# Kernel tuning notes

Hardware: AMD Instinct MI355X
Metric: run time of the kernel (lower is better)

The kernel has to match this reference:

```python
import jax, jax.numpy as jnp
import numpy as np

B, K, H, W = 16, 32, 28, 28   # batch, set size, image h, image w
HID, OUT = 64, 64             # hid_dim, out_dim
NOPS = 8                      # permutation-equivariant 3->3 pool/broadcast basis ops


def setup_inputs() -> dict:
    key = jax.random.key(0)
    ks = jax.random.split(key, 8)
    def p(k, shape, fan_in):
        return jax.random.normal(k, shape, jnp.float32) / np.float32(np.sqrt(fan_in))
    return dict(
        x=jax.random.normal(ks[0], (B, K, H, W), jnp.float32),
        conv1_w=p(ks[1], (32, 1, 3, 3), 9),
        conv1_b=jnp.zeros((32,), jnp.float32),
        conv2_w=p(ks[2], (64, 32, 3, 3), 32 * 9),
        conv2_b=jnp.zeros((64,), jnp.float32),
        fc_w=p(ks[3], (HID, 64 * 7 * 7), 64 * 7 * 7),
        fc_b=jnp.zeros((HID,), jnp.float32),
        eq_w=p(ks[4], (HID, OUT, NOPS), HID * NOPS),
        eq_b=jnp.zeros((OUT,), jnp.float32),
        out_w=p(ks[5], (1, OUT), OUT),
        out_b=jnp.zeros((1,), jnp.float32),
    )


def _conv2d(x, w, b):
    y = jax.lax.conv_general_dilated(x, w, (1, 1), 'SAME',
                                     dimension_numbers=('NCHW', 'OIHW', 'NCHW'))
    return y + b[None, :, None, None]


def _maxpool2(x):
    return jax.lax.reduce_window(x, -jnp.inf, jax.lax.max,
                                 (1, 1, 2, 2), (1, 1, 2, 2), 'VALID')


def _forward(x, conv1_w, conv1_b, conv2_w, conv2_b, fc_w, fc_b, eq_w, eq_b, out_w, out_b):
    # --- BasicConvNet embed: (B*K, 1, H, W) -> (B*K, HID) ---
    x1 = x.reshape(B * K, 1, H, W)
    h1 = _maxpool2(jax.nn.relu(_conv2d(x1, conv1_w, conv1_b)))   # (B*K, 32, 14, 14)
    h2 = _maxpool2(jax.nn.relu(_conv2d(h1, conv2_w, conv2_b)))   # (B*K, 64, 7, 7)
    feat = jax.nn.relu(h2.reshape(B * K, -1) @ fc_w.T + fc_b)    # (B*K, HID)
    x4 = feat.reshape(B, K, HID)

    # --- triple outer product: (B, HID, K, K, K), no contracted index ---
    x5 = jnp.einsum('bid,bjd,bkd->bdijk', x4, x4, x4)

    # --- SetEq3to3: 8 equivariant pool/broadcast basis ops, contracted with eq_w[d,e,o].
    # Contract each pooled tensor with its slice of eq_w BEFORE broadcasting (same math,
    # avoids materializing 8 full (B,d,K,K,K) op tensors). ---
    m_i  = x5.mean(2)           # (B, d, j, k)
    m_j  = x5.mean(3)           # (B, d, i, k)
    m_k  = x5.mean(4)           # (B, d, i, j)
    m_ij = m_i.mean(2)          # (B, d, k)
    m_ik = m_i.mean(3)          # (B, d, j)
    m_jk = m_j.mean(3)          # (B, d, i)
    m_all = m_ij.mean(2)        # (B, d)

    x6 = (jnp.einsum('bdijk,de->beijk', x5, eq_w[:, :, 0])
          + jnp.einsum('bdjk,de->bejk', m_i, eq_w[:, :, 1])[:, :, None, :, :]
          + jnp.einsum('bdik,de->beik', m_j, eq_w[:, :, 2])[:, :, :, None, :]
          + jnp.einsum('bdij,de->beij', m_k, eq_w[:, :, 3])[:, :, :, :, None]
          + jnp.einsum('bdk,de->bek', m_ij, eq_w[:, :, 4])[:, :, None, None, :]
          + jnp.einsum('bdj,de->bej', m_ik, eq_w[:, :, 5])[:, :, None, :, None]
          + jnp.einsum('bdi,de->bei', m_jk, eq_w[:, :, 6])[:, :, :, None, None]
          + jnp.einsum('bd,de->be', m_all, eq_w[:, :, 7])[:, :, None, None, None]
          + eq_b[None, :, None, None, None])          # (B, OUT, K, K, K)

    # permute to channels-last, relu, pool over (i,j,k), relu, final linear
    x7 = jax.nn.relu(x6.transpose(0, 2, 3, 4, 1))     # (B, K, K, K, OUT)
    x8 = x7.mean(axis=(1, 2, 3))                      # (B, OUT)
    x9 = jax.nn.relu(x8)
    # dropout_prob = 0 -> identity
    return x9 @ out_w.T + out_b                       # (B, 1)


def reference(x, conv1_w, conv1_b, conv2_w, conv2_b, fc_w, fc_b, eq_w, eq_b, out_w, out_b):
    return _forward(x, conv1_w, conv1_b, conv2_w, conv2_b, fc_w, fc_b,
                    eq_w, eq_b, out_w, out_b)
```

## Files before the change

kernel.cpp:

```cpp
#include <hip/hip_runtime.h>
#include <hip/hip_bf16.h>


typedef __attribute__((ext_vector_type(8))) short short8;
typedef __attribute__((ext_vector_type(4))) float f32x4;

__device__ __forceinline__ f32x4 mfma_bf16(short8 a, short8 b, f32x4 c) {
  return __builtin_amdgcn_mfma_f32_16x16x32_bf16(a, b, c, 0, 0, 0);
}

__device__ __forceinline__ unsigned short f2bs(float f) {
  unsigned int u = __float_as_uint(f);
  unsigned int r = u + 0x7fffu + ((u >> 16) & 1u);
  return (unsigned short)(r >> 16);
}
__device__ __forceinline__ unsigned int pk2(float x, float y) {
  union { __hip_bfloat162 h; unsigned int u; } cv;
  cv.h = __float22bfloat162_rn(make_float2(x, y));
  return cv.u;
}
__device__ __forceinline__ void ub8(const short* p, float* f) {
  uint4 u = *(const uint4*)p;
  f[0] = __uint_as_float(u.x << 16); f[1] = __uint_as_float(u.x & 0xffff0000u);
  f[2] = __uint_as_float(u.y << 16); f[3] = __uint_as_float(u.y & 0xffff0000u);
  f[4] = __uint_as_float(u.z << 16); f[5] = __uint_as_float(u.z & 0xffff0000u);
  f[6] = __uint_as_float(u.w << 16); f[7] = __uint_as_float(u.w & 0xffff0000u);
}

__global__ __launch_bounds__(256) void k0_prep(const float* __restrict__ eqw,
    const float* __restrict__ w2, const float* __restrict__ fcw,
    float* __restrict__ W7t, short* __restrict__ Wtb,
    short* __restrict__ w2p, short* __restrict__ fcwb) {
  const int b = blockIdx.x, t = threadIdx.x;
  if (b < 8) {
    const int m = b;
    for (int idx = t; idx < 4096; idx += 256) {
      int e = idx >> 6, d = idx & 63;
      float v = eqw[d*512 + e*8 + m];
      if (m == 7) W7t[idx] = v;
      else        Wtb[m*4096 + idx] = (short)f2bs(v);
    }
  } else if (b == 8) {
    for (int idx = t; idx < 18432; idx += 256) {
      int s2 = idx & 7, c = (idx >> 3) & 63, quad = (idx >> 9) & 3, dd = idx >> 11;
      w2p[idx] = (short)f2bs(w2[c*288 + (quad*8 + s2)*9 + dd]);
    }
  } else {
    int base = (b - 9)*12544 + t;
    for (int q = 0; q < 49; ++q) {
      int idx = base + q*256;
      fcwb[idx] = (short)f2bs(fcw[idx]);
    }
  }
}

__global__ __launch_bounds__(256, 2) void kA_conv(const float* __restrict__ x,
    const float* __restrict__ w1, const float* __restrict__ b1,
    const short* __restrict__ w2p, const float* __restrict__ b2,
    const short* __restrict__ fcwb, const float* __restrict__ fcb,
    float* __restrict__ feat) {
  const int n = blockIdx.x, t = threadIdx.x;
  __shared__ float si[30*30];
  __shared__ float sw[32*9];
  __shared__ float sb[32];
  __shared__ __align__(16) short inT[16*18*40];
  __shared__ __align__(16) float h2f[3136];
  __shared__ float sf4[256];
  const int wv = t >> 6, l = t & 63, quad = l >> 4, col = l & 15;

  const int c_out = wv*16 + col;
  short8 Bq[9];
  {
    const short8* wp = (const short8*)w2p + quad*64 + c_out;
#pragma unroll
    for (int dd = 0; dd < 9; ++dd) Bq[dd] = wp[dd*256];
  }
  const float bb2 = b2[c_out];

  for (int idx = t; idx < 900; idx += 256) si[idx] = 0.f;
  {
    unsigned int* zp = (unsigned int*)inT;
    for (int idx = t; idx < 5760; idx += 256) zp[idx] = 0u;
  }
  for (int idx = t; idx < 288; idx += 256) sw[idx] = w1[idx];
  if (t < 32) sb[t] = b1[t];
  __syncthreads();
  for (int idx = t; idx < 784; idx += 256) {
    int y = idx / 28, xx = idx - y*28;
    si[(y+1)*30 + xx + 1] = x[n*784 + idx];
  }
  __syncthreads();

  {
    const int cg = t & 7;
    float wreg[4][9], breg[4];
#pragma unroll
    for (int cc = 0; cc < 4; ++cc) {
      breg[cc] = sb[cg*4 + cc];
#pragma unroll
      for (int q = 0; q < 9; ++q) wreg[cc][q] = sw[(cg*4 + cc)*9 + q];
    }
    for (int idx = t; idx < 1568; idx += 256) {
      int pos = idx >> 3;
      int py = pos / 14, px = pos - py*14;
      float pt[4][4];
#pragma unroll
      for (int r = 0; r < 4; ++r)
#pragma unroll
        for (int q = 0; q < 4; ++q)
          pt[r][q] = si[(2*py + r)*30 + 2*px + q];
      float res[4];
#pragma unroll
      for (int cc = 0; cc < 4; ++cc) {
        float best = 0.f;
#pragma unroll
        for (int a = 0; a < 2; ++a)
#pragma unroll
          for (int b3 = 0; b3 < 2; ++b3) {
            float v = breg[cc]
              + wreg[cc][0]*pt[a+0][b3+0] + wreg[cc][1]*pt[a+0][b3+1] + wreg[cc][2]*pt[a+0][b3+2]
              + wreg[cc][3]*pt[a+1][b3+0] + wreg[cc][4]*pt[a+1][b3+1] + wreg[cc][5]*pt[a+1][b3+2]
              + wreg[cc][6]*pt[a+2][b3+0] + wreg[cc][7]*pt[a+2][b3+1] + wreg[cc][8]*pt[a+2][b3+2];
            best = fmaxf(best, v);
          }
        res[cc] = best;
      }
      uint2 pkd;
      pkd.x = pk2(res[0], res[1]);
      pkd.y = pk2(res[2], res[3]);
      *(uint2*)&inT[(py+1)*720 + (px+1)*40 + cg*4] = pkd;
    }
  }
  __syncthreads();

  for (int p = 0; p < 7; ++p) {
    short8 Ar[4][3];
#pragma unroll
    for (int rr = 0; rr < 4; ++rr)
#pragma unroll
      for (int dx = 0; dx < 3; ++dx)
        Ar[rr][dx] = *(const short8*)&inT[(2*p + rr)*720 + (col + dx)*40 + quad*8];
    f32x4 a0 = {0.f,0.f,0.f,0.f}, a1 = {0.f,0.f,0.f,0.f};
#pragma unroll
    for (int dy = 0; dy < 3; ++dy)
#pragma unroll
      for (int dx = 0; dx < 3; ++dx) {
        a0 = mfma_bf16(Ar[dy][dx],     Bq[dy*3 + dx], a0);
        a1 = mfma_bf16(Ar[dy + 1][dx], Bq[dy*3 + dx], a1);
      }
#pragma unroll
    for (int a = 0; a < 2; ++a) {
      int px = quad*2 + a;
      if (px < 7) {
        float m0 = fmaxf(fmaxf(a0[2*a], a0[2*a + 1]), fmaxf(a1[2*a], a1[2*a + 1]));
        h2f[c_out*49 + p*7 + px] = fmaxf(m0 + bb2, 0.f);
      }
    }
  }
  {
    const short* Wrow = fcwb + l*3136 + wv*784;
    const float* Hrow = h2f + wv*784;
    float a0 = 0.f, a1 = 0.f, a2 = 0.f, a3 = 0.f;
#pragma unroll 7
    for (int j = 0; j < 98; ++j) {
      float wf[8]; ub8(&Wrow[j*8], wf);
      float4 hx = *(const float4*)&Hrow[j*8];
      float4 hy = *(const float4*)&Hrow[j*8 + 4];
      a0 += wf[0]*hx.x + wf[4]*hy.x;
      a1 += wf[1]*hx.y + wf[5]*hy.y;
      a2 += wf[2]*hx.z + wf[6]*hy.z;
      a3 += wf[3]*hx.w + wf[7]*hy.w;
    }
    sf4[wv*64 + l] = (a0 + a1) + (a2 + a3);
  }
  __syncthreads();
  if (t < 64) {
    float v = sf4[t] + sf4[64 + t] + sf4[128 + t] + sf4[192 + t] + fcb[t];
    feat[n*64 + t] = fmaxf(v, 0.f);
  }
}

__global__ __launch_bounds__(256, 2) void k5_mfma(const float* __restrict__ feat,
    const short* __restrict__ Wtb, const float* __restrict__ W7t,
    const float* __restrict__ eqb, float* __restrict__ x8p) {
  __shared__ __align__(16) float Fm[32*68];
  __shared__ __align__(16) float FI[64];
  __shared__ __align__(16) float SV[64];
  __shared__ __align__(16) float SC[64];
  __shared__ __align__(16) float TC[64];
  __shared__ __align__(16) float C0[64];
  __shared__ float C0P[128];
  __shared__ float KCf[32*68];
  __shared__ float JCf[32*68];
  __shared__ float RED[256];
  __shared__ __align__(16) short Fb[32*72];
  __shared__ __align__(16) short QPb[64*72];
  __shared__ __align__(16) short G2b[64*72];
  __shared__ __align__(16) short G3b[64*72];

  const int i = blockIdx.x, b = blockIdx.y, t = threadIdx.x;
  const int w = t >> 6, l = t & 63, quad = l >> 4, col = l & 15;

  for (int idx = t; idx < 2048; idx += 256) {
    int r = idx >> 6, d = idx & 63;
    float v = feat[b*2048 + idx];
    Fm[r*68 + d] = v;
    Fb[r*72 + d] = (short)f2bs(v);
  }
  if (t < 64) FI[t] = feat[b*2048 + i*64 + t];
  __syncthreads();

  if (t < 64) {
    float a = 0.f;
#pragma unroll
    for (int r = 0; r < 32; ++r) a += Fm[r*68 + t];
    a *= (1.f/32.f);
    SV[t] = a;
    SC[t] = a*a*a;
  }
  __syncthreads();

  if (t < 64) {
    const float* W7 = W7t + t*64;
    float acc = 0.f;
#pragma unroll
    for (int d = 0; d < 64; d += 4) {
      float4 w4 = *(const float4*)&W7[d];
      acc += SC[d]*w4.x + SC[d+1]*w4.y + SC[d+2]*w4.z + SC[d+3]*w4.w;
    }
    TC[t] = acc + eqb[t];
  }

  {
    const int e = t >> 2, dbase = (t & 3) * 16;
#pragma unroll
    for (int h = 0; h < 2; ++h) {
      int off = dbase + h*8;
      float w0[8], w1r[8], w2r[8], w3r[8], w4r[8], w5r[8];
      ub8(&Wtb[0*4096 + e*64 + off], w0);
      ub8(&Wtb[1*4096 + e*64 + off], w1r);
      ub8(&Wtb[2*4096 + e*64 + off], w2r);
      ub8(&Wtb[3*4096 + e*64 + off], w3r);
      ub8(&Wtb[4*4096 + e*64 + off], w4r);
      ub8(&Wtb[5*4096 + e*64 + off], w5r);
      uint4 qv, g2v, g3v;
      unsigned int* qp = &qv.x;
      unsigned int* g2p = &g2v.x;
      unsigned int* g3p = &g3v.x;
#pragma unroll
      for (int j = 0; j < 4; ++j) {
        float fi0 = FI[off + 2*j],     fi1 = FI[off + 2*j + 1];
        float s0  = SV[off + 2*j],     s1  = SV[off + 2*j + 1];
        float q0 = fi0*w0[2*j]   + s0*w1r[2*j];
        float q1 = fi1*w0[2*j+1] + s1*w1r[2*j+1];
        float a0 = s0*(fi0*w2r[2*j]   + s0*w4r[2*j]);
        float a1 = s1*(fi1*w2r[2*j+1] + s1*w4r[2*j+1]);
        float c0 = s0*(fi0*w3r[2*j]   + s0*w5r[2*j]);
        float c1 = s1*(fi1*w3r[2*j+1] + s1*w5r[2*j+1]);
        qp[j]  = pk2(q0, q1);
        g2p[j] = pk2(a0, a1);
        g3p[j] = pk2(c0, c1);
      }
      *(uint4*)&QPb[e*72 + off] = qv;
      *(uint4*)&G2b[e*72 + off] = g2v;
      *(uint4*)&G3b[e*72 + off] = g3v;
    }
  }
  if (t < 128) {
    int e = t & 63, dh = t >> 6;
    const short* W6 = Wtb + 6*4096 + e*64 + dh*32;
    float a = 0.f;
#pragma unroll
    for (int g = 0; g < 4; ++g) {
      float wf[8];
      ub8(&W6[g*8], wf);
#pragma unroll
      for (int dd = 0; dd < 8; ++dd) {
        int d = dh*32 + g*8 + dd;
        float sd = SV[d];
        a += sd*sd*FI[d]*wf[dd];
      }
    }
    C0P[dh*64 + e] = a;
  }
  __syncthreads();

  if (w < 2) {
    const short* G = w ? G3b : G2b;
    float* DST = w ? JCf : KCf;
    short8 Bf[4][2];
#pragma unroll
    for (int n = 0; n < 4; ++n)
#pragma unroll
      for (int s2 = 0; s2 < 2; ++s2)
        Bf[n][s2] = *(const short8*)&G[(n*16 + col)*72 + s2*32 + quad*8];
#pragma unroll
    for (int m = 0; m < 2; ++m) {
      short8 A0 = *(const short8*)&Fb[(m*16 + col)*72 + quad*8];
      short8 A1 = *(const short8*)&Fb[(m*16 + col)*72 + 32 + quad*8];
#pragma unroll
      for (int n = 0; n < 4; ++n) {
        f32x4 z = {0.f, 0.f, 0.f, 0.f};
        f32x4 ac = mfma_bf16(A1, Bf[n][1], mfma_bf16(A0, Bf[n][0], z));
#pragma unroll
        for (int r = 0; r < 4; ++r)
          DST[(m*16 + quad*4 + r)*68 + n*16 + col] = ac[r];
      }
    }
  } else if (w == 2) {
    C0[l] = C0P[l] + C0P[64 + l] + TC[l];
  }
  __syncthreads();

  float c0v[4];
#pragma unroll
  for (int n = 0; n < 4; ++n) c0v[n] = C0[n*16 + col];
  float jcq[8][4];
#pragma unroll
  for (int jj = 0; jj < 8; ++jj)
#pragma unroll
    for (int n = 0; n < 4; ++n)
      jcq[jj][n] = JCf[(w*8 + jj)*68 + n*16 + col] + c0v[n];
  float kcv[2][4][4];
#pragma unroll
  for (int kb2 = 0; kb2 < 2; ++kb2)
#pragma unroll
    for (int r = 0; r < 4; ++r)
#pragma unroll
      for (int n = 0; n < 4; ++n)
        kcv[kb2][r][n] = KCf[(kb2*16 + quad*4 + r)*68 + n*16 + col];
  short8 Bq[4][2];
#pragma unroll
  for (int n = 0; n < 4; ++n)
#pragma unroll
    for (int s2 = 0; s2 < 2; ++s2)
      Bq[n][s2] = *(const short8*)&QPb[(n*16 + col)*72 + s2*32 + quad*8];

  float4 fkv[2][4];
#pragma unroll
  for (int kb2 = 0; kb2 < 2; ++kb2) {
    const float* fk = &Fm[(kb2*16 + col)*68 + quad*8];
    fkv[kb2][0] = *(const float4*)(fk);
    fkv[kb2][1] = *(const float4*)(fk + 4);
    fkv[kb2][2] = *(const float4*)(fk + 32);
    fkv[kb2][3] = *(const float4*)(fk + 36);
  }

  float sum[4] = {0.f, 0.f, 0.f, 0.f};
  union SU { short8 v; unsigned int u[4]; };

#pragma unroll
  for (int jj = 0; jj < 8; ++jj) {
    const float* fj = &Fm[(w*8 + jj)*68 + quad*8];
    float4 j0 = *(const float4*)(fj);
    float4 j1 = *(const float4*)(fj + 4);
    float4 j2 = *(const float4*)(fj + 32);
    float4 j3 = *(const float4*)(fj + 36);
#pragma unroll
    for (int kb2 = 0; kb2 < 2; ++kb2) {
      float4 k0 = fkv[kb2][0], k1 = fkv[kb2][1];
      float4 k2v = fkv[kb2][2], k3v = fkv[kb2][3];
      SU A0, A1;
      A0.u[0] = pk2(j0.x*k0.x, j0.y*k0.y);
      A0.u[1] = pk2(j0.z*k0.z, j0.w*k0.w);
      A0.u[2] = pk2(j1.x*k1.x, j1.y*k1.y);
      A0.u[3] = pk2(j1.z*k1.z, j1.w*k1.w);
      A1.u[0] = pk2(j2.x*k2v.x, j2.y*k2v.y);
      A1.u[1] = pk2(j2.z*k2v.z, j2.w*k2v.w);
      A1.u[2] = pk2(j3.x*k3v.x, j3.y*k3v.y);
      A1.u[3] = pk2(j3.z*k3v.z, j3.w*k3v.w);
      f32x4 ac[4];
#pragma unroll
      for (int n = 0; n < 4; ++n) {
        f32x4 z = {0.f, 0.f, 0.f, 0.f};
        ac[n] = mfma_bf16(A1.v, Bq[n][1], mfma_bf16(A0.v, Bq[n][0], z));
      }
#pragma unroll
      for (int n = 0; n < 4; ++n)
#pragma unroll
        for (int r = 0; r < 4; ++r) {
          float v = ac[n][r] + kcv[kb2][r][n] + jcq[jj][n];
          sum[n] += fmaxf(v, 0.f);
        }
    }
  }

#pragma unroll
  for (int n = 0; n < 4; ++n) {
    float v = sum[n];
    v += __shfl_xor(v, 16, 64);
    v += __shfl_xor(v, 32, 64);
    if (l < 16) RED[w*64 + n*16 + l] = v;
  }
  __syncthreads();
  if (t < 64) {
    float tot = RED[t] + RED[64 + t] + RED[128 + t] + RED[192 + t];
    x8p[(b*32 + i)*64 + t] = tot;
  }
}

__global__ __launch_bounds__(64) void k6_out(const float* __restrict__ x8p,
    const float* __restrict__ ow, const float* __restrict__ ob,
    float* __restrict__ out) {
  const int bb = blockIdx.x, t = threadIdx.x;
  float a = 0.f;
#pragma unroll
  for (int i = 0; i < 32; ++i) a += x8p[(bb*32 + i)*64 + t];
  float v = fmaxf(a * (1.f/32768.f), 0.f) * ow[t];
#pragma unroll
  for (int off = 32; off > 0; off >>= 1) v += __shfl_down(v, off, 64);
  if (t == 0) out[bb] = v + ob[0];
}

extern "C" void kernel_launch(void* const* d_in, const int* in_sizes, int n_in,
                              void* d_out, int out_size, void* d_ws, size_t ws_size,
                              hipStream_t stream) {
  const float* x   = (const float*)d_in[0];
  const float* c1w = (const float*)d_in[1];
  const float* c1b = (const float*)d_in[2];
  const float* c2w = (const float*)d_in[3];
  const float* c2b = (const float*)d_in[4];
  const float* fcw = (const float*)d_in[5];
  const float* fcb = (const float*)d_in[6];
  const float* eqw = (const float*)d_in[7];
  const float* eqb = (const float*)d_in[8];
  const float* ow  = (const float*)d_in[9];
  const float* ob  = (const float*)d_in[10];
  float* out = (float*)d_out;

  float* feat = (float*)d_ws;
  float* x8p  = feat + 32768;
  float* W7t  = x8p + 32768;
  short* Wtb  = (short*)(W7t + 4096);
  short* w2p  = Wtb + 28672;
  short* fcwb = w2p + 18432;
  (void)in_sizes; (void)n_in; (void)out_size; (void)ws_size;

  hipLaunchKernelGGL(k0_prep, dim3(25), dim3(256), 0, stream,
                     eqw, c2w, fcw, W7t, Wtb, w2p, fcwb);
  hipLaunchKernelGGL(kA_conv, dim3(512), dim3(256), 0, stream,
                     x, c1w, c1b, w2p, c2b, fcwb, fcb, feat);
  hipLaunchKernelGGL(k5_mfma, dim3(32, 16), dim3(256), 0, stream,
                     feat, Wtb, W7t, eqb, x8p);
  hipLaunchKernelGGL(k6_out,  dim3(16),  dim3(64),  0, stream, x8p, ow, ob, out);
}
```

Before: 138.9 us.

## Transpose FC weights for coalesced loads and hoist set-mean/op7 term into separate kernel

The prep kernel now stores the bf16 FC weight transposed (k-major, output-minor), so each lane group in the FC stage reads contiguous 8-output chunks and broadcasts one activation, reducing across lanes with xor shuffles instead of striding 3136 elements per lane. A new small kernel computes the per-batch set mean and the constant op-7 contribution once per batch rather than in each of the 32 blocks per batch of the equivariant kernel, which drops two barriers and redundant work there. This adds one more kernel launch and a global round-trip for those small vectors, and a non-coalesced strided read from fcw in prep.

```diff
diff --git a/kernel.cpp b/kernel.cpp
--- a/kernel.cpp
+++ b/kernel.cpp
@@ -30,7 +30,7 @@
 __global__ __launch_bounds__(256) void k0_prep(const float* __restrict__ eqw,
     const float* __restrict__ w2, const float* __restrict__ fcw,
     float* __restrict__ W7t, short* __restrict__ Wtb,
-    short* __restrict__ w2p, short* __restrict__ fcwb) {
+    short* __restrict__ w2p, short* __restrict__ fcwt) {
   const int b = blockIdx.x, t = threadIdx.x;
   if (b < 8) {
     const int m = b;
@@ -49,7 +49,8 @@
     int base = (b - 9)*12544 + t;
     for (int q = 0; q < 49; ++q) {
       int idx = base + q*256;
-      fcwb[idx] = (short)f2bs(fcw[idx]);
+      int k = idx >> 6, e = idx & 63;
+      fcwt[idx] = (short)f2bs(fcw[e*3136 + k]);
     }
   }
 }
@@ -57,7 +58,7 @@
 __global__ __launch_bounds__(256, 2) void kA_conv(const float* __restrict__ x,
     const float* __restrict__ w1, const float* __restrict__ b1,
     const short* __restrict__ w2p, const float* __restrict__ b2,
-    const short* __restrict__ fcwb, const float* __restrict__ fcb,
+    const short* __restrict__ fcwt, const float* __restrict__ fcb,
     float* __restrict__ feat) {
   const int n = blockIdx.x, t = threadIdx.x;
   __shared__ float si[30*30];
@@ -158,20 +159,27 @@
     }
   }
   {
-    const short* Wrow = fcwb + l*3136 + wv*784;
-    const float* Hrow = h2f + wv*784;
-    float a0 = 0.f, a1 = 0.f, a2 = 0.f, a3 = 0.f;
+    const int g = l >> 3, s = l & 7;
+    const short* Wp = fcwt + (wv*784 + g)*64 + s*8;
+    const float* Hp = h2f + wv*784 + g;
+    float acc[8] = {0.f,0.f,0.f,0.f,0.f,0.f,0.f,0.f};
 #pragma unroll 7
     for (int j = 0; j < 98; ++j) {
-      float wf[8]; ub8(&Wrow[j*8], wf);
-      float4 hx = *(const float4*)&Hrow[j*8];
-      float4 hy = *(const float4*)&Hrow[j*8 + 4];
-      a0 += wf[0]*hx.x + wf[4]*hy.x;
-      a1 += wf[1]*hx.y + wf[5]*hy.y;
-      a2 += wf[2]*hx.z + wf[6]*hy.z;
-      a3 += wf[3]*hx.w + wf[7]*hy.w;
-    }
-    sf4[wv*64 + l] = (a0 + a1) + (a2 + a3);
+      float wf[8]; ub8(Wp + j*512, wf);
+      float hk = Hp[j*8];
+#pragma unroll
+      for (int q = 0; q < 8; ++q) acc[q] += wf[q] * hk;
+    }
+#pragma unroll
+    for (int q = 0; q < 8; ++q) {
+      acc[q] += __shfl_xor(acc[q], 8, 64);
+      acc[q] += __shfl_xor(acc[q], 16, 64);
+      acc[q] += __shfl_xor(acc[q], 32, 64);
+    }
+    if (g == 0) {
+#pragma unroll
+      for (int q = 0; q < 8; ++q) sf4[wv*64 + s*8 + q] = acc[q];
+    }
   }
   __syncthreads();
   if (t < 64) {
@@ -180,14 +188,41 @@
   }
 }
 
+__global__ __launch_bounds__(256) void k4b(const float* __restrict__ feat,
+    const float* __restrict__ W7t, const float* __restrict__ eqb,
+    float* __restrict__ s, float* __restrict__ t7c) {
+  __shared__ __align__(16) float sf[2048];
+  __shared__ float ss[64];
+  const int b = blockIdx.x, t = threadIdx.x;
+  for (int v4 = t; v4 < 512; v4 += 256)
+    *(float4*)&sf[v4*4] = *(const float4*)&feat[b*2048 + v4*4];
+  __syncthreads();
+  if (t < 64) {
+    float a = 0.f;
+#pragma unroll
+    for (int r = 0; r < 32; ++r) a += sf[r*64 + t];
+    a *= (1.f/32.f);
+    s[b*64 + t] = a;
+    ss[t] = a;
+  }
+  __syncthreads();
+  if (t < 64) {
+    const float* W7 = W7t + t*64;
+    float t7 = 0.f;
+    for (int d = 0; d < 64; ++d) {
+      float sv = ss[d];
+      t7 += sv*sv*sv * W7[d];
+    }
+    t7c[b*64 + t] = t7 + eqb[t];
+  }
+}
+
 __global__ __launch_bounds__(256, 2) void k5_mfma(const float* __restrict__ feat,
-    const short* __restrict__ Wtb, const float* __restrict__ W7t,
-    const float* __restrict__ eqb, float* __restrict__ x8p) {
+    const float* __restrict__ s_, const short* __restrict__ Wtb,
+    const float* __restrict__ t7c, float* __restrict__ x8p) {
   __shared__ __align__(16) float Fm[32*68];
   __shared__ __align__(16) float FI[64];
   __shared__ __align__(16) float SV[64];
-  __shared__ __align__(16) float SC[64];
-  __shared__ __align__(16) float TC[64];
   __shared__ __align__(16) float C0[64];
   __shared__ float C0P[128];
   __shared__ float KCf[32*68];
@@ -207,42 +242,21 @@
     Fm[r*68 + d] = v;
     Fb[r*72 + d] = (short)f2bs(v);
   }
-  if (t < 64) FI[t] = feat[b*2048 + i*64 + t];
-  __syncthreads();
-
-  if (t < 64) {
-    float a = 0.f;
-#pragma unroll
-    for (int r = 0; r < 32; ++r) a += Fm[r*68 + t];
-    a *= (1.f/32.f);
-    SV[t] = a;
-    SC[t] = a*a*a;
-  }
-  __syncthreads();
-
-  if (t < 64) {
-    const float* W7 = W7t + t*64;
-    float acc = 0.f;
-#pragma unroll
-    for (int d = 0; d < 64; d += 4) {
-      float4 w4 = *(const float4*)&W7[d];
-      acc += SC[d]*w4.x + SC[d+1]*w4.y + SC[d+2]*w4.z + SC[d+3]*w4.w;
-    }
-    TC[t] = acc + eqb[t];
-  }
+  if (t < 64) { FI[t] = feat[b*2048 + i*64 + t]; SV[t] = s_[b*64 + t]; }
+  __syncthreads();
 
   {
     const int e = t >> 2, dbase = (t & 3) * 16;
 #pragma unroll
     for (int h = 0; h < 2; ++h) {
       int off = dbase + h*8;
-      float w0[8], w1r[8], w2r[8], w3r[8], w4r[8], w5r[8];
+      float w0[8], w1[8], w2[8], w3[8], w4[8], w5[8];
       ub8(&Wtb[0*4096 + e*64 + off], w0);
-      ub8(&Wtb[1*4096 + e*64 + off], w1r);
-      ub8(&Wtb[2*4096 + e*64 + off], w2r);
-      ub8(&Wtb[3*4096 + e*64 + off], w3r);
-      ub8(&Wtb[4*4096 + e*64 + off], w4r);
-      ub8(&Wtb[5*4096 + e*64 + off], w5r);
+      ub8(&Wtb[1*4096 + e*64 + off], w1);
+      ub8(&Wtb[2*4096 + e*64 + off], w2);
+      ub8(&Wtb[3*4096 + e*64 + off], w3);
+      ub8(&Wtb[4*4096 + e*64 + off], w4);
+      ub8(&Wtb[5*4096 + e*64 + off], w5);
       uint4 qv, g2v, g3v;
       unsigned int* qp = &qv.x;
       unsigned int* g2p = &g2v.x;
@@ -251,12 +265,12 @@
       for (int j = 0; j < 4; ++j) {
         float fi0 = FI[off + 2*j],     fi1 = FI[off + 2*j + 1];
         float s0  = SV[off + 2*j],     s1  = SV[off + 2*j + 1];
-        float q0 = fi0*w0[2*j]   + s0*w1r[2*j];
-        float q1 = fi1*w0[2*j+1] + s1*w1r[2*j+1];
-        float a0 = s0*(fi0*w2r[2*j]   + s0*w4r[2*j]);
-        float a1 = s1*(fi1*w2r[2*j+1] + s1*w4r[2*j+1]);
-        float c0 = s0*(fi0*w3r[2*j]   + s0*w5r[2*j]);
-        float c1 = s1*(fi1*w3r[2*j+1] + s1*w5r[2*j+1]);
+        float q0 = fi0*w0[2*j]   + s0*w1[2*j];
+        float q1 = fi1*w0[2*j+1] + s1*w1[2*j+1];
+        float a0 = s0*(fi0*w2[2*j]   + s0*w4[2*j]);
+        float a1 = s1*(fi1*w2[2*j+1] + s1*w4[2*j+1]);
+        float c0 = s0*(fi0*w3[2*j]   + s0*w5[2*j]);
+        float c1 = s1*(fi1*w3[2*j+1] + s1*w5[2*j+1]);
         qp[j]  = pk2(q0, q1);
         g2p[j] = pk2(a0, a1);
         g3p[j] = pk2(c0, c1);
@@ -308,7 +322,7 @@
       }
     }
   } else if (w == 2) {
-    C0[l] = C0P[l] + C0P[64 + l] + TC[l];
+    C0[l] = C0P[l] + C0P[64 + l] + t7c[b*64 + l];
   }
   __syncthreads();
 
@@ -433,14 +447,18 @@
   float* W7t  = x8p + 32768;
   short* Wtb  = (short*)(W7t + 4096);
   short* w2p  = Wtb + 28672;
-  short* fcwb = w2p + 18432;
+  short* fcwt = w2p + 18432;
+  float* s    = (float*)(fcwt + 200704);
+  float* t7c  = s + 1024;
   (void)in_sizes; (void)n_in; (void)out_size; (void)ws_size;
 
   hipLaunchKernelGGL(k0_prep, dim3(25), dim3(256), 0, stream,
-                     eqw, c2w, fcw, W7t, Wtb, w2p, fcwb);
+                     eqw, c2w, fcw, W7t, Wtb, w2p, fcwt);
   hipLaunchKernelGGL(kA_conv, dim3(512), dim3(256), 0, stream,
-                     x, c1w, c1b, w2p, c2b, fcwb, fcb, feat);
+                     x, c1w, c1b, w2p, c2b, fcwt, fcb, feat);
+  hipLaunchKernelGGL(k4b,     dim3(16),  dim3(256), 0, stream,
+                     feat, W7t, eqb, s, t7c);
   hipLaunchKernelGGL(k5_mfma, dim3(32, 16), dim3(256), 0, stream,
-                     feat, Wtb, W7t, eqb, x8p);
+                     feat, s, Wtb, t7c, x8p);
   hipLaunchKernelGGL(k6_out,  dim3(16),  dim3(64),  0, stream, x8p, ow, ob, out);
 }
```

New measurement: 127.2 us, median of 2. 8.4% less time.
